# Performance work log

Measured on AMD Instinct MI355X. Metric: run time of the kernel, lower is better.

The kernel has to match this reference:

```python
import jax, jax.numpy as jnp
import numpy as np

POOL = 7; SR = 2; SCALE = 1.0 / 16
NUM_CLASSES = 21
NMS_THR = 0.5; MIN_SIZE = 1.0; TOPK = 100; SCORE_THR = 0.05
BBOX_CLIP = float(np.log(1000.0 / 16))


def roi_align(feat, rois):
    # feat: [C,H,W]; rois: [P,4] xyxy in image coords. torchvision aligned=True, sampling_ratio=2.
    C, H, W = feat.shape
    S = POOL * SR
    x0r = rois[:, 0] * SCALE - 0.5
    y0r = rois[:, 1] * SCALE - 0.5
    bw = (rois[:, 2] - rois[:, 0]) * SCALE / POOL
    bh = (rois[:, 3] - rois[:, 1]) * SCALE / POOL
    t = (jnp.arange(S, dtype=feat.dtype) + 0.5) / SR  # sample offsets in bin units
    ys = y0r[:, None] + bh[:, None] * t  # [P,S]
    xs = x0r[:, None] + bw[:, None] * t  # [P,S]
    vy = (ys >= -1.0) & (ys <= H)
    vx = (xs >= -1.0) & (xs <= W)
    y = jnp.clip(ys, 0.0, H - 1)
    x = jnp.clip(xs, 0.0, W - 1)
    yl = jnp.floor(y).astype(jnp.int32); xl = jnp.floor(x).astype(jnp.int32)
    yh = jnp.minimum(yl + 1, H - 1);     xh = jnp.minimum(xl + 1, W - 1)
    ly = y - yl; lx = x - xl
    hy = 1.0 - ly; hx = 1.0 - lx

    def g(Yi, Xi):  # -> [C,P,S,S]
        return feat[:, Yi[:, :, None], Xi[:, None, :]]

    val = (g(yl, xl) * (hy[:, :, None] * hx[:, None, :])
         + g(yl, xh) * (hy[:, :, None] * lx[:, None, :])
         + g(yh, xl) * (ly[:, :, None] * hx[:, None, :])
         + g(yh, xh) * (ly[:, :, None] * lx[:, None, :]))
    val = val * (vy[:, :, None] & vx[:, None, :])[None].astype(feat.dtype)
    P = rois.shape[0]
    val = val.reshape(C, P, POOL, SR, POOL, SR).mean(axis=(3, 5))  # avg over 2x2 samples/bin
    return val.transpose(1, 0, 2, 3)  # [P,C,POOL,POOL]


def decode(pred, proposals):
    # pred: [N,K,4] (dx,dy,dw,dh); proposals: [N,4]
    w = proposals[:, 2] - proposals[:, 0]
    h = proposals[:, 3] - proposals[:, 1]
    cx = proposals[:, 0] + 0.5 * w
    cy = proposals[:, 1] + 0.5 * h
    dx, dy = pred[..., 0], pred[..., 1]
    dw = jnp.minimum(pred[..., 2], BBOX_CLIP)
    dh = jnp.minimum(pred[..., 3], BBOX_CLIP)
    pcx = dx * w[:, None] + cx[:, None]
    pcy = dy * h[:, None] + cy[:, None]
    pw = jnp.exp(dw) * w[:, None]
    ph = jnp.exp(dh) * h[:, None]
    return jnp.stack([pcx - 0.5 * pw, pcy - 0.5 * ph, pcx + 0.5 * pw, pcy + 0.5 * ph], axis=-1)


def box_iou(b):
    x1, y1, x2, y2 = b[:, 0], b[:, 1], b[:, 2], b[:, 3]
    area = (x2 - x1) * (y2 - y1)
    iw = jnp.maximum(jnp.minimum(x2[:, None], x2[None, :]) - jnp.maximum(x1[:, None], x1[None, :]), 0.0)
    ih = jnp.maximum(jnp.minimum(y2[:, None], y2[None, :]) - jnp.maximum(y1[:, None], y1[None, :]), 0.0)
    inter = iw * ih
    return inter / (area[:, None] + area[None, :] - inter)


def filter_predictions(boxes, labels, scores):
    # score threshold + min-size + per-class greedy NMS + topK, static shapes (padded to TOPK)
    N = scores.shape[0]
    ws = boxes[:, 2] - boxes[:, 0]
    hs = boxes[:, 3] - boxes[:, 1]
    valid = (scores > SCORE_THR) & (ws >= MIN_SIZE) & (hs >= MIN_SIZE)
    skey = jnp.where(valid, scores, -jnp.inf)
    order = jnp.argsort(-skey)
    b = boxes[order]; s = skey[order]; l = labels[order]; v = valid[order]
    # batched_nms via per-class coordinate offset
    off = jax.lax.stop_gradient(jnp.max(boxes) + 1.0)
    ob = jax.lax.stop_gradient(b) + (l.astype(b.dtype) * off)[:, None]
    iou = box_iou(ob)  # [N,N]
    idx = jnp.arange(N)

    def body(keep, i):
        sup = (iou[i] > NMS_THR) & keep[i] & (idx > i)
        return keep & ~sup, None

    keep, _ = jax.lax.scan(body, v, idx)
    rank = jnp.cumsum(keep) - 1
    final = keep & (rank < TOPK)
    pick = jnp.argsort(jnp.where(final, idx, N))[:TOPK]  # kept indices in score order, padded
    ok = final[pick]
    out_boxes = jnp.where(ok[:, None], b[pick], 0.0)
    out_scores = jnp.where(ok, s[pick], 0.0)
    out_labels = jnp.where(ok, l[pick], -1)
    return out_boxes, out_labels, out_scores


def roi_head_forward(image, feat, proposals, fc6_w, fc6_b, fc7_w, fc7_b, cls_w, cls_b, reg_w, reg_b):
    H_img, W_img = image.shape[-2], image.shape[-1]
    pooled = roi_align(feat[0], proposals)  # [P,C,7,7]
    x = pooled.reshape(pooled.shape[0], -1)
    x = jax.nn.relu(x @ fc6_w.T + fc6_b)
    x = jax.nn.relu(x @ fc7_w.T + fc7_b)
    cls_scores = x @ cls_w.T + cls_b                       # [P,K]
    box_pred = (x @ reg_w.T + reg_b).reshape(-1, NUM_CLASSES, 4)
    boxes = decode(box_pred, proposals)                    # [P,K,4]
    scores = jax.nn.softmax(cls_scores, axis=-1)
    boxes = jnp.stack([boxes[..., 0].clip(0, W_img), boxes[..., 1].clip(0, H_img),
                       boxes[..., 2].clip(0, W_img), boxes[..., 3].clip(0, H_img)], axis=-1)
    labels = jnp.broadcast_to(jnp.arange(NUM_CLASSES), scores.shape)
    boxes = boxes[:, 1:].reshape(-1, 4)
    scores = scores[:, 1:].reshape(-1)
    labels = (labels[:, 1:] - 1).reshape(-1)
    return filter_predictions(boxes, labels, scores)


def setup_inputs() -> dict:
    key = jax.random.key(0)
    ks = jax.random.split(key, 12)
    H_img, W_img = 800, 1072
    P, C = 300, 512
    image = jnp.zeros((1, 3, H_img, W_img), jnp.float32)
    feat = jax.random.normal(ks[0], (1, C, H_img // 16, W_img // 16), jnp.float32)
    cx = jax.random.uniform(ks[1], (P,)) * W_img
    cy = jax.random.uniform(ks[2], (P,)) * H_img
    bw = 20.0 + jax.random.uniform(ks[3], (P,)) * 300.0
    bh = 20.0 + jax.random.uniform(ks[4], (P,)) * 300.0
    proposals = jnp.stack([jnp.clip(cx - bw / 2, 0, W_img), jnp.clip(cy - bh / 2, 0, H_img),
                           jnp.clip(cx + bw / 2, 0, W_img), jnp.clip(cy + bh / 2, 0, H_img)], axis=1)
    fin = C * POOL * POOL  # 25088
    D = 1024
    fc6_w = jax.random.normal(ks[5], (D, fin), jnp.float32) / np.sqrt(fin)
    fc6_b = jnp.zeros((D,), jnp.float32)
    fc7_w = jax.random.normal(ks[6], (D, D), jnp.float32) / np.sqrt(D)
    fc7_b = jnp.zeros((D,), jnp.float32)
    cls_w = jax.random.normal(ks[7], (NUM_CLASSES, D), jnp.float32) / np.sqrt(D)
    cls_b = jnp.zeros((NUM_CLASSES,), jnp.float32)
    reg_w = jax.random.normal(ks[8], (NUM_CLASSES * 4, D), jnp.float32) * 0.001
    reg_b = jnp.zeros((NUM_CLASSES * 4,), jnp.float32)
    return {"image": image, "feat": feat, "proposals": proposals,
            "fc6_w": fc6_w, "fc6_b": fc6_b, "fc7_w": fc7_w, "fc7_b": fc7_b,
            "cls_w": cls_w, "cls_b": cls_b, "reg_w": reg_w, "reg_b": reg_b}


def reference(image, feat, proposals, fc6_w, fc6_b, fc7_w, fc7_b, cls_w, cls_b, reg_w, reg_b):
    return roi_head_forward(image, feat, proposals, fc6_w, fc6_b, fc7_w, fc7_b, cls_w, cls_b, reg_w, reg_b)
```

## Files before the change

### kernel.cpp

```cpp
#include <hip/hip_runtime.h>
#include <hip/hip_bf16.h>
#include <math.h>

#define P_N   300
#define C_N   512
#define H_F   50
#define W_F   67
#define HW_F  3350
#define D_N   1024
#define FIN   25088
#define NCLS  21
#define NCAND 6000
#define W_IMG 1072.0f
#define H_IMG 800.0f
#define BBOX_CLIP_F 4.135166556742356f
#define KS6   42
#define STEPS6_PER_Z 19
#define KS7   16
#define STEPS7_PER_Z 2
#define KSH   16
#define STEPSH_PER_Z 2
#define NHEAD 128
#define NW    96
#define LO_SCALE 2048.0f
#define LO_INV   (1.0f/2048.0f)

typedef __attribute__((ext_vector_type(8)))  _Float16 half8;
typedef __attribute__((ext_vector_type(16))) float    f32x16;

__device__ __forceinline__ void split16(float f, _Float16& h, _Float16& l) {
  h = (_Float16)f;
  l = (_Float16)((f - (float)h) * LO_SCALE);
}

__global__ __launch_bounds__(256) void transpose_feat(const float* __restrict__ feat,
                                                      float* __restrict__ ft) {
  __shared__ float tile[32][33];
  const int s0 = blockIdx.x * 32, c0 = blockIdx.y * 32;
  const int tx = threadIdx.x, ty = threadIdx.y;
  for (int r = ty; r < 32; r += 8) {
    int c = c0 + r, s = s0 + tx;
    tile[r][tx] = (s < HW_F) ? feat[(size_t)c * HW_F + s] : 0.0f;
  }
  __syncthreads();
  for (int r = ty; r < 32; r += 8) {
    int s = s0 + r, c = c0 + tx;
    if (s < HW_F) ft[(size_t)s * C_N + c] = tile[tx][r];
  }
}

__global__ __launch_bounds__(256) void roi_align_k(const float* __restrict__ ft,
                                                   const float* __restrict__ rois,
                                                   _Float16* __restrict__ Xhi,
                                                   _Float16* __restrict__ Xlo) {
  __shared__ _Float16 hbuf[12544] __attribute__((aligned(16)));
  __shared__ _Float16 lbuf[12544] __attribute__((aligned(16)));
  __shared__ int   g_yl[14], g_yh[14], g_xl[14], g_xh[14];
  __shared__ float g_ly[14], g_hy[14], g_lx[14], g_hx[14];
  __shared__ int   g_vy[14], g_vx[14];

  const int p   = blockIdx.x;
  const int ch  = blockIdx.y;
  const int tid = threadIdx.x;

  if (tid < 14) {
    const float rx0 = rois[p*4+0], ry0 = rois[p*4+1], rx1 = rois[p*4+2], ry1 = rois[p*4+3];
    const float x0r = rx0 * 0.0625f - 0.5f;
    const float y0r = ry0 * 0.0625f - 0.5f;
    const float bw  = (rx1 - rx0) * 0.0625f * (1.0f / 7.0f);
    const float bh  = (ry1 - ry0) * 0.0625f * (1.0f / 7.0f);
    const float t   = ((float)tid + 0.5f) * 0.5f;

    const float ys = y0r + bh * t;
    g_vy[tid] = (ys >= -1.0f) && (ys <= (float)H_F);
    float y = fminf(fmaxf(ys, 0.0f), (float)(H_F - 1));
    int yi = (int)floorf(y);
    g_yl[tid] = yi; g_yh[tid] = min(yi + 1, H_F - 1);
    g_ly[tid] = y - (float)yi; g_hy[tid] = 1.0f - (y - (float)yi);

    const float xs = x0r + bw * t;
    g_vx[tid] = (xs >= -1.0f) && (xs <= (float)W_F);
    float x = fminf(fmaxf(xs, 0.0f), (float)(W_F - 1));
    int xi = (int)floorf(x);
    g_xl[tid] = xi; g_xh[tid] = min(xi + 1, W_F - 1);
    g_lx[tid] = x - (float)xi; g_hx[tid] = 1.0f - (x - (float)xi);
  }
  __syncthreads();

  const int c = ch * 256 + tid;
  for (int cell = 0; cell < 49; ++cell) {
    const int py = cell / 7;
    const int px = cell - py * 7;
    float acc = 0.0f;
#pragma unroll
    for (int sy = 0; sy < 2; ++sy) {
      const int iy = 2 * py + sy;
      if (!g_vy[iy]) continue;
      const float ly = g_ly[iy], hy = g_hy[iy];
      const int ry0i = g_yl[iy] * W_F, ry1i = g_yh[iy] * W_F;
#pragma unroll
      for (int sx = 0; sx < 2; ++sx) {
        const int ix = 2 * px + sx;
        if (!g_vx[ix]) continue;
        const float lx = g_lx[ix], hx = g_hx[ix];
        const float* b00 = ft + (size_t)(ry0i + g_xl[ix]) * C_N;
        const float* b01 = ft + (size_t)(ry0i + g_xh[ix]) * C_N;
        const float* b10 = ft + (size_t)(ry1i + g_xl[ix]) * C_N;
        const float* b11 = ft + (size_t)(ry1i + g_xh[ix]) * C_N;
        acc += (hy*hx)*b00[c] + (hy*lx)*b01[c] + (ly*hx)*b10[c] + (ly*lx)*b11[c];
      }
    }
    _Float16 h, l;
    split16(acc * 0.25f, h, l);
    hbuf[tid * 49 + cell] = h;
    lbuf[tid * 49 + cell] = l;
  }
  __syncthreads();

  const size_t base = (size_t)p * FIN + (size_t)ch * 12544;
  const uint4* hs = (const uint4*)hbuf;
  const uint4* ls = (const uint4*)lbuf;
  uint4* dh = (uint4*)(Xhi + base);
  uint4* dl = (uint4*)(Xlo + base);
  for (int k = tid; k < 1568; k += 256) { dh[k] = hs[k]; dl[k] = ls[k]; }
}

__device__ __forceinline__ int swz(int slot, int ks) {
  return slot ^ ((slot >> 5) & 1) ^ (((slot >> 3) & 1) << 1) ^ ((ks & 1) << 2);
}

__global__ __launch_bounds__(256, 2) void gemm_f16_3p(
    const _Float16* __restrict__ Ahi, const _Float16* __restrict__ Alo,
    const float* __restrict__ Wt, float* __restrict__ Pt,
    int M, int K, int steps_per_z, int ldc)
{
  __shared__ _Float16 lds[16384];
  const int tid  = threadIdx.x;
  const int lane = tid & 63, wave = tid >> 6;
  const int wm = wave >> 1, wn = wave & 1;

  const int GX = gridDim.x, GY = gridDim.y;
  const int T  = GX * GY * gridDim.z;
  int flat = blockIdx.x + GX * (blockIdx.y + GY * blockIdx.z);
  if ((T & 7) == 0) flat = (flat & 7) * (T >> 3) + (flat >> 3);
  const int bx = flat % GX;
  const int by = (flat / GX) % GY;
  const int bz = flat / (GX * GY);

  const int m0 = bx * 128, n0 = by * 128;
  const int steps_total = K >> 5;
  const int s0 = bz * steps_per_z;
  const int s1 = min(s0 + steps_per_z, steps_total);

  f32x16 acc0[2][2], acc1[2][2];
#pragma unroll
  for (int a = 0; a < 2; ++a)
#pragma unroll
    for (int b = 0; b < 2; ++b) {
#pragma unroll
      for (int r = 0; r < 16; ++r) { acc0[a][b][r] = 0.f; acc1[a][b][r] = 0.f; }
    }

  const int srow = tid >> 2;
  const int j8   = tid & 3;
  const int ksW  = j8 >> 1, kc8 = j8 & 1;
  const int wslot = swz((kc8 << 5) | (srow & 31), ksW);

  for (int step = s0; step < s1; ++step) {
    const int kb = step << 5;
#pragma unroll
    for (int half = 0; half < 2; ++half) {
      const int row = srow + half * 64;
      const int mf  = row >> 5;
      const int gm  = m0 + row;
      uint4 vh = make_uint4(0,0,0,0), vl = make_uint4(0,0,0,0);
      if (gm < M) {
        vh = *reinterpret_cast<const uint4*>(Ahi + (size_t)gm * K + kb + j8 * 8);
        vl = *reinterpret_cast<const uint4*>(Alo + (size_t)gm * K + kb + j8 * 8);
      }
      const int base = (mf * 2 + ksW) * 512 + wslot * 8;
      *reinterpret_cast<uint4*>(&lds[base])        = vh;
      *reinterpret_cast<uint4*>(&lds[4096 + base]) = vl;
    }
#pragma unroll
    for (int half = 0; half < 2; ++half) {
      const int n = srow + half * 64;
      const float* wp = Wt + (size_t)(n0 + n) * K + kb + j8 * 8;
      const float4 f0 = *reinterpret_cast<const float4*>(wp);
      const float4 f1 = *reinterpret_cast<const float4*>(wp + 4);
      float fv[8] = {f0.x, f0.y, f0.z, f0.w, f1.x, f1.y, f1.z, f1.w};
      union { _Float16 h[8]; uint4 v; } uh, ul;
#pragma unroll
      for (int e = 0; e < 8; ++e) split16(fv[e], uh.h[e], ul.h[e]);
      const int nf = n >> 5;
      const int base = 8192 + (nf * 2 + ksW) * 512 + wslot * 8;
      *reinterpret_cast<uint4*>(&lds[base])        = uh.v;
      *reinterpret_cast<uint4*>(&lds[4096 + base]) = ul.v;
    }
    __syncthreads();
#pragma unroll
    for (int ks = 0; ks < 2; ++ks) {
      const int rslot = swz(lane, ks) * 8;
      half8 ah[2], al[2], bh[2], bl[2];
#pragma unroll
      for (int mi = 0; mi < 2; ++mi) {
        const int mf = wm * 2 + mi;
        ah[mi] = *reinterpret_cast<const half8*>(&lds[(mf * 2 + ks) * 512 + rslot]);
        al[mi] = *reinterpret_cast<const half8*>(&lds[4096 + (mf * 2 + ks) * 512 + rslot]);
      }
#pragma unroll
      for (int ni = 0; ni < 2; ++ni) {
        const int nf = wn * 2 + ni;
        bh[ni] = *reinterpret_cast<const half8*>(&lds[8192  + (nf * 2 + ks) * 512 + rslot]);
        bl[ni] = *reinterpret_cast<const half8*>(&lds[12288 + (nf * 2 + ks) * 512 + rslot]);
      }
#pragma unroll
      for (int mi = 0; mi < 2; ++mi)
#pragma unroll
        for (int ni = 0; ni < 2; ++ni) {
          acc0[mi][ni] = __builtin_amdgcn_mfma_f32_32x32x16_f16(ah[mi], bh[ni], acc0[mi][ni], 0, 0, 0);
          acc1[mi][ni] = __builtin_amdgcn_mfma_f32_32x32x16_f16(ah[mi], bl[ni], acc1[mi][ni], 0, 0, 0);
          acc1[mi][ni] = __builtin_amdgcn_mfma_f32_32x32x16_f16(al[mi], bh[ni], acc1[mi][ni], 0, 0, 0);
        }
    }
    __syncthreads();
  }
  const int col = lane & 31, rhi = lane >> 5;
  float* outp = Pt + (size_t)bz * ((size_t)M * ldc);
#pragma unroll
  for (int mi = 0; mi < 2; ++mi)
#pragma unroll
    for (int ni = 0; ni < 2; ++ni) {
      const int n = n0 + (wn * 2 + ni) * 32 + col;
      if (n >= ldc) continue;
#pragma unroll
      for (int r = 0; r < 16; ++r) {
        const int m = m0 + (wm * 2 + mi) * 32 + ((r & 3) + 8 * (r >> 2) + 4 * rhi);
        if (m < M) outp[(size_t)m * ldc + n] = acc0[mi][ni][r] + acc1[mi][ni][r] * LO_INV;
      }
    }
}

__global__ __launch_bounds__(256) void reduce_bias(
    const float* __restrict__ Pt, const float* __restrict__ bias,
    float* __restrict__ out_f32, _Float16* __restrict__ out_hi, _Float16* __restrict__ out_lo,
    int MN, int KS, int nmask, int relu)
{
  int i = blockIdx.x * 256 + threadIdx.x;
  if (i >= MN) return;
  float s = 0.0f;
  for (int k = 0; k < KS; ++k) s += Pt[(size_t)k * MN + i];
  s += bias[i & nmask];
  if (relu) s = fmaxf(s, 0.0f);
  if (out_f32) out_f32[i] = s;
  if (out_hi) {
    _Float16 h, l; split16(s, h, l);
    out_hi[i] = h; out_lo[i] = l;
  }
}

__global__ __launch_bounds__(256) void prep_head(const float* __restrict__ cls_w,
                                                 const float* __restrict__ cls_b,
                                                 const float* __restrict__ reg_w,
                                                 const float* __restrict__ reg_b,
                                                 float* __restrict__ Wpad,
                                                 float* __restrict__ bpad) {
  const int row = blockIdx.x;
  const int t = threadIdx.x;
  const float* src = (row < NCLS) ? (cls_w + (size_t)row * D_N)
                   : (row < 105)  ? (reg_w + (size_t)(row - NCLS) * D_N) : nullptr;
  float4 v = make_float4(0.f, 0.f, 0.f, 0.f);
  if (src) v = reinterpret_cast<const float4*>(src)[t];
  reinterpret_cast<float4*>(Wpad + (size_t)row * D_N)[t] = v;
  if (t == 0)
    bpad[row] = (row < NCLS) ? cls_b[row] : (row < 105) ? reg_b[row - NCLS] : 0.0f;
}

__global__ __launch_bounds__(64) void decode_kernel(const float* __restrict__ logits,
                                                    const float* __restrict__ props,
                                                    float* __restrict__ cboxes,
                                                    float* __restrict__ cscores,
                                                    int* __restrict__ cvalid) {
  const int p = blockIdx.x;
  const int lane = threadIdx.x;
  const float* lg = logits + (size_t)p * NHEAD;

  float s = (lane < NCLS) ? lg[lane] : -__builtin_inff();
  float mx = s;
#pragma unroll
  for (int off = 32; off > 0; off >>= 1) mx = fmaxf(mx, __shfl_xor(mx, off));
  float e = (lane < NCLS) ? expf(s - mx) : 0.0f;
  float sum = e;
#pragma unroll
  for (int off = 32; off > 0; off >>= 1) sum += __shfl_xor(sum, off);
  const float sm = e / sum;

  if (lane >= 1 && lane < NCLS) {
    const int c = lane;
    const float x0 = props[p*4+0], y0 = props[p*4+1], x1 = props[p*4+2], y1 = props[p*4+3];
    const float w = x1 - x0, hh = y1 - y0;
    const float cx = x0 + 0.5f * w, cy = y0 + 0.5f * hh;
    const float dx = lg[NCLS + c*4 + 0];
    const float dy = lg[NCLS + c*4 + 1];
    const float dw = fminf(lg[NCLS + c*4 + 2], BBOX_CLIP_F);
    const float dh = fminf(lg[NCLS + c*4 + 3], BBOX_CLIP_F);
    const float pcx = dx * w + cx, pcy = dy * hh + cy;
    const float pw = expf(dw) * w, ph = expf(dh) * hh;
    float bx0 = pcx - 0.5f * pw, by0 = pcy - 0.5f * ph;
    float bx1 = pcx + 0.5f * pw, by1 = pcy + 0.5f * ph;
    bx0 = fminf(fmaxf(bx0, 0.0f), W_IMG);
    by0 = fminf(fmaxf(by0, 0.0f), H_IMG);
    bx1 = fminf(fmaxf(bx1, 0.0f), W_IMG);
    by1 = fminf(fmaxf(by1, 0.0f), H_IMG);
    const int idx = p * 20 + (c - 1);
    cboxes[idx*4+0] = bx0; cboxes[idx*4+1] = by0;
    cboxes[idx*4+2] = bx1; cboxes[idx*4+3] = by1;
    const bool valid = (sm > 0.05f) && ((bx1 - bx0) >= 1.0f) && ((by1 - by0) >= 1.0f);
    cscores[idx] = sm;
    cvalid[idx] = valid ? 1 : 0;
  }
}

__global__ void zero_counter(int* c) { if (threadIdx.x == 0 && blockIdx.x == 0) *c = 0; }

__global__ __launch_bounds__(256) void compact_kernel(const float* __restrict__ cscores,
                                                      const int* __restrict__ cvalid,
                                                      unsigned long long* __restrict__ ckeys,
                                                      int* __restrict__ vcount) {
  int i = blockIdx.x * 256 + threadIdx.x;
  if (i >= NCAND) return;
  if (cvalid[i]) {
    int pos = atomicAdd(vcount, 1);
    unsigned u = __float_as_uint(cscores[i]);
    ckeys[pos] = ((unsigned long long)(~u) << 32) | (unsigned)i;
  }
}

__global__ __launch_bounds__(1024) void sort_gather(const unsigned long long* __restrict__ ckeys,
                                                    const int* __restrict__ vcount,
                                                    const float* __restrict__ cboxes,
                                                    float4* __restrict__ sbox,
                                                    float* __restrict__ sscore,
                                                    int* __restrict__ slab) {
  __shared__ unsigned long long keys[8192];
  const int tid = threadIdx.x;
  const int V = *vcount;
  int Npad = 64; while (Npad < V) Npad <<= 1;
  for (int i = tid; i < Npad; i += 1024)
    keys[i] = (i < V) ? ckeys[i] : ~0ULL;
  __syncthreads();
  for (int kk = 2; kk <= Npad; kk <<= 1) {
    for (int j = kk >> 1; j > 0; j >>= 1) {
      for (int i = tid; i < Npad; i += 1024) {
        int ij = i ^ j;
        if (ij > i) {
          unsigned long long a = keys[i], b = keys[ij];
          bool up = ((i & kk) == 0);
          if ((a > b) == up) { keys[i] = b; keys[ij] = a; }
        }
      }
      __syncthreads();
    }
  }
  for (int i = tid; i < V; i += 1024) {
    unsigned long long key = keys[i];
    int idx = (int)(key & 0xffffffffu);
    sbox[i]   = *reinterpret_cast<const float4*>(&cboxes[(size_t)idx * 4]);
    sscore[i] = __uint_as_float(~(unsigned)(key >> 32));
    slab[i]   = idx % 20;
  }
}

__global__ __launch_bounds__(256) void iou_matrix(const float4* __restrict__ sbox,
                                                  const int* __restrict__ slab,
                                                  const int* __restrict__ vcount,
                                                  unsigned long long* __restrict__ mask) {
  const int V = *vcount;
  const int i = blockIdx.x * 4 + (threadIdx.x >> 6);
  const int lane = threadIdx.x & 63;
  if (i >= V) return;
  const float4 bi = sbox[i];
  const int li = slab[i];
  const float ai = (bi.z - bi.x) * (bi.w - bi.y);
  const int nw = (V + 63) >> 6;
  for (int w = 0; w < nw; ++w) {
    const int j = (w << 6) + lane;
    bool sup = false;
    if (j > i && j < V && slab[j] == li) {
      const float4 bj = sbox[j];
      const float iw = fminf(bi.z, bj.z) - fmaxf(bi.x, bj.x);
      const float ih = fminf(bi.w, bj.w) - fmaxf(bi.y, bj.y);
      const float inter = fmaxf(iw, 0.0f) * fmaxf(ih, 0.0f);
      const float aj = (bj.z - bj.x) * (bj.w - bj.y);
      sup = inter / (ai + aj - inter) > 0.5f;
    }
    const unsigned long long m = __ballot(sup);
    if (lane == 0) mask[(size_t)i * NW + w] = m;
  }
}

__global__ __launch_bounds__(64) void nms_scan(const float4* __restrict__ sbox,
                                               const float* __restrict__ sscore,
                                               const int* __restrict__ slab,
                                               const int* __restrict__ vcount,
                                               const unsigned long long* __restrict__ mask,
                                               float* __restrict__ out) {
  const int lane = threadIdx.x;
  const int V = min(*vcount, NCAND);
  unsigned long long live0 = ~0ULL, live1 = ~0ULL;
  int nk = 0;
  for (int i = 0; i < V && nk < 100; ++i) {
    const int wi = i >> 6, bi = i & 63;
    union { unsigned long long u; uint2 v; } t;
    t.u = (wi < 64) ? live0 : live1;
    const int src = (wi < 64) ? wi : (wi - 64);
    const unsigned lo = __shfl(t.v.x, src);
    const unsigned hi = __shfl(t.v.y, src);
    const unsigned long long wv = ((unsigned long long)hi << 32) | lo;
    if ((wv >> bi) & 1ULL) {
      if (lane == 0) {
        const float4 bb = sbox[i];
        out[nk*4+0] = bb.x; out[nk*4+1] = bb.y; out[nk*4+2] = bb.z; out[nk*4+3] = bb.w;
        out[400 + nk] = (float)slab[i];
        out[500 + nk] = sscore[i];
      }
      const unsigned long long* mrow = mask + (size_t)i * NW;
      live0 &= ~mrow[lane];
      if (lane < NW - 64) live1 &= ~mrow[64 + lane];
      nk++;
    }
  }
  for (int r = nk + lane; r < 100; r += 64) {
    out[r*4+0] = 0.0f; out[r*4+1] = 0.0f; out[r*4+2] = 0.0f; out[r*4+3] = 0.0f;
    out[400 + r] = -1.0f;
    out[500 + r] = 0.0f;
  }
}

extern "C" void kernel_launch(void* const* d_in, const int* in_sizes, int n_in,
                              void* d_out, int out_size, void* d_ws, size_t ws_size,
                              hipStream_t stream) {
  const float* feat   = (const float*)d_in[1];
  const float* props  = (const float*)d_in[2];
  const float* fc6_w  = (const float*)d_in[3];
  const float* fc6_b  = (const float*)d_in[4];
  const float* fc7_w  = (const float*)d_in[5];
  const float* fc7_b  = (const float*)d_in[6];
  const float* cls_w  = (const float*)d_in[7];
  const float* cls_b  = (const float*)d_in[8];
  const float* reg_w  = (const float*)d_in[9];
  const float* reg_b  = (const float*)d_in[10];

  char* ws = (char*)d_ws;
  size_t off = 0;
  auto alloc = [&](size_t bytes) -> void* {
    void* p = ws + off;
    off += (bytes + 255) & ~(size_t)255;
    return p;
  };

  _Float16* Xhi  = (_Float16*)alloc((size_t)P_N * FIN * 2);
  _Float16* Xlo  = (_Float16*)alloc((size_t)P_N * FIN * 2);
  float*    Pt   = (float*)alloc((size_t)KS6 * P_N * D_N * 4);
  _Float16* h6hi = (_Float16*)alloc((size_t)P_N * D_N * 2);
  _Float16* h6lo = (_Float16*)alloc((size_t)P_N * D_N * 2);
  _Float16* h7hi = (_Float16*)alloc((size_t)P_N * D_N * 2);
  _Float16* h7lo = (_Float16*)alloc((size_t)P_N * D_N * 2);
  float*    Wpad = (float*)alloc((size_t)NHEAD * D_N * 4);
  float*    bpad = (float*)alloc((size_t)NHEAD * 4);
  float*  logits = (float*)alloc((size_t)P_N * NHEAD * 4);
  float*  cboxes = (float*)alloc((size_t)NCAND * 4 * 4);
  float* cscores = (float*)alloc((size_t)NCAND * 4);
  int*    cvalid = (int*)alloc((size_t)NCAND * 4);
  unsigned long long* ckeys = (unsigned long long*)alloc((size_t)NCAND * 8);
  float4*   sbox = (float4*)alloc((size_t)NCAND * 16);
  float*  sscore = (float*)alloc((size_t)NCAND * 4);
  int*      slab = (int*)alloc((size_t)NCAND * 4);
  unsigned long long* supmask = (unsigned long long*)alloc((size_t)NCAND * NW * 8);
  int*    vcount = (int*)alloc(256);
  float* ft = Pt;
  (void)ws_size; (void)in_sizes; (void)n_in; (void)out_size;

  prep_head<<<NHEAD, 256, 0, stream>>>(cls_w, cls_b, reg_w, reg_b, Wpad, bpad);
  transpose_feat<<<dim3((HW_F + 31) / 32, C_N / 32), dim3(32, 8), 0, stream>>>(feat, ft);
  roi_align_k<<<dim3(P_N, 2), 256, 0, stream>>>(ft, props, Xhi, Xlo);
  gemm_f16_3p<<<dim3(3, 8, KS6), 256, 0, stream>>>(Xhi, Xlo, fc6_w, Pt, P_N, FIN, STEPS6_PER_Z, D_N);
  reduce_bias<<<(P_N * D_N + 255) / 256, 256, 0, stream>>>(
      Pt, fc6_b, nullptr, h6hi, h6lo, P_N * D_N, KS6, D_N - 1, 1);
  gemm_f16_3p<<<dim3(3, 8, KS7), 256, 0, stream>>>(h6hi, h6lo, fc7_w, Pt, P_N, D_N, STEPS7_PER_Z, D_N);
  reduce_bias<<<(P_N * D_N + 255) / 256, 256, 0, stream>>>(
      Pt, fc7_b, nullptr, h7hi, h7lo, P_N * D_N, KS7, D_N - 1, 1);
  gemm_f16_3p<<<dim3(3, 1, KSH), 256, 0, stream>>>(h7hi, h7lo, Wpad, Pt, P_N, D_N, STEPSH_PER_Z, NHEAD);
  reduce_bias<<<(P_N * NHEAD + 255) / 256, 256, 0, stream>>>(
      Pt, bpad, logits, nullptr, nullptr, P_N * NHEAD, KSH, NHEAD - 1, 0);
  decode_kernel<<<P_N, 64, 0, stream>>>(logits, props, cboxes, cscores, cvalid);
  zero_counter<<<1, 1, 0, stream>>>(vcount);
  compact_kernel<<<(NCAND + 255) / 256, 256, 0, stream>>>(cscores, cvalid, ckeys, vcount);
  sort_gather<<<1, 1024, 0, stream>>>(ckeys, vcount, cboxes, sbox, sscore, slab);
  iou_matrix<<<(NCAND + 3) / 4, 256, 0, stream>>>(sbox, slab, vcount, supmask);
  nms_scan<<<1, 64, 0, stream>>>(sbox, sscore, slab, vcount, supmask, (float*)d_out);
}
```

Before: 344.9 us.

## Merge split-fp16 accumulators, fuse compaction into decode, speed NMS scan

The split-fp16 GEMM now pre-scales the A and B operands so that the hi and lo cross products can share a single accumulator set. This halves accumulator registers and lets launch bounds ask for 3 blocks per CU. Candidate compaction and the counter reset are folded into decode_kernel and prep_head, which removes two kernel launches and the intermediate score and valid buffers. nms_scan now walks only live bits with ffs and reads only the mask words it needs. The risks are reduced accuracy from fp16 range/scaling choices and a nondeterministic candidate order when atomics are used inside decode, which the sort should absorb.

```diff
diff --git a/kernel.cpp b/kernel.cpp
--- a/kernel.cpp
+++ b/kernel.cpp
@@ -22,15 +22,17 @@
 #define STEPSH_PER_Z 2
 #define NHEAD 128
 #define NW    96
-#define LO_SCALE 2048.0f
-#define LO_INV   (1.0f/2048.0f)
+#define A_SCALE 16.0f
+#define B_SCALE 256.0f
+#define O_SCALE (1.0f / 4096.0f)
 
 typedef __attribute__((ext_vector_type(8)))  _Float16 half8;
 typedef __attribute__((ext_vector_type(16))) float    f32x16;
 
-__device__ __forceinline__ void split16(float f, _Float16& h, _Float16& l) {
-  h = (_Float16)f;
-  l = (_Float16)((f - (float)h) * LO_SCALE);
+__device__ __forceinline__ void splitA(float f, _Float16& h, _Float16& l) {
+  float fs = f * A_SCALE;
+  h = (_Float16)fs;
+  l = (_Float16)(fs - (float)h);
 }
 
 __global__ __launch_bounds__(256) void transpose_feat(const float* __restrict__ feat,
@@ -111,7 +113,7 @@
       }
     }
     _Float16 h, l;
-    split16(acc * 0.25f, h, l);
+    splitA(acc * 0.25f, h, l);
     hbuf[tid * 49 + cell] = h;
     lbuf[tid * 49 + cell] = l;
   }
@@ -129,7 +131,7 @@
   return slot ^ ((slot >> 5) & 1) ^ (((slot >> 3) & 1) << 1) ^ ((ks & 1) << 2);
 }
 
-__global__ __launch_bounds__(256, 2) void gemm_f16_3p(
+__global__ __launch_bounds__(256, 3) void gemm_f16_3p(
     const _Float16* __restrict__ Ahi, const _Float16* __restrict__ Alo,
     const float* __restrict__ Wt, float* __restrict__ Pt,
     int M, int K, int steps_per_z, int ldc)
@@ -152,14 +154,13 @@
   const int s0 = bz * steps_per_z;
   const int s1 = min(s0 + steps_per_z, steps_total);
 
-  f32x16 acc0[2][2], acc1[2][2];
+  f32x16 acc[2][2];
 #pragma unroll
   for (int a = 0; a < 2; ++a)
 #pragma unroll
-    for (int b = 0; b < 2; ++b) {
-#pragma unroll
-      for (int r = 0; r < 16; ++r) { acc0[a][b][r] = 0.f; acc1[a][b][r] = 0.f; }
-    }
+    for (int b = 0; b < 2; ++b)
+#pragma unroll
+      for (int r = 0; r < 16; ++r) acc[a][b][r] = 0.f;
 
   const int srow = tid >> 2;
   const int j8   = tid & 3;
@@ -191,7 +192,11 @@
       float fv[8] = {f0.x, f0.y, f0.z, f0.w, f1.x, f1.y, f1.z, f1.w};
       union { _Float16 h[8]; uint4 v; } uh, ul;
 #pragma unroll
-      for (int e = 0; e < 8; ++e) split16(fv[e], uh.h[e], ul.h[e]);
+      for (int e = 0; e < 8; ++e) {
+        float fs = fv[e] * B_SCALE;
+        uh.h[e] = (_Float16)fs;
+        ul.h[e] = (_Float16)(fs - (float)uh.h[e]);
+      }
       const int nf = n >> 5;
       const int base = 8192 + (nf * 2 + ksW) * 512 + wslot * 8;
       *reinterpret_cast<uint4*>(&lds[base])        = uh.v;
@@ -218,9 +223,9 @@
       for (int mi = 0; mi < 2; ++mi)
 #pragma unroll
         for (int ni = 0; ni < 2; ++ni) {
-          acc0[mi][ni] = __builtin_amdgcn_mfma_f32_32x32x16_f16(ah[mi], bh[ni], acc0[mi][ni], 0, 0, 0);
-          acc1[mi][ni] = __builtin_amdgcn_mfma_f32_32x32x16_f16(ah[mi], bl[ni], acc1[mi][ni], 0, 0, 0);
-          acc1[mi][ni] = __builtin_amdgcn_mfma_f32_32x32x16_f16(al[mi], bh[ni], acc1[mi][ni], 0, 0, 0);
+          acc[mi][ni] = __builtin_amdgcn_mfma_f32_32x32x16_f16(ah[mi], bh[ni], acc[mi][ni], 0, 0, 0);
+          acc[mi][ni] = __builtin_amdgcn_mfma_f32_32x32x16_f16(ah[mi], bl[ni], acc[mi][ni], 0, 0, 0);
+          acc[mi][ni] = __builtin_amdgcn_mfma_f32_32x32x16_f16(al[mi], bh[ni], acc[mi][ni], 0, 0, 0);
         }
     }
     __syncthreads();
@@ -236,7 +241,7 @@
 #pragma unroll
       for (int r = 0; r < 16; ++r) {
         const int m = m0 + (wm * 2 + mi) * 32 + ((r & 3) + 8 * (r >> 2) + 4 * rhi);
-        if (m < M) outp[(size_t)m * ldc + n] = acc0[mi][ni][r] + acc1[mi][ni][r] * LO_INV;
+        if (m < M) outp[(size_t)m * ldc + n] = acc[mi][ni][r] * O_SCALE;
       }
     }
 }
@@ -254,7 +259,7 @@
   if (relu) s = fmaxf(s, 0.0f);
   if (out_f32) out_f32[i] = s;
   if (out_hi) {
-    _Float16 h, l; split16(s, h, l);
+    _Float16 h, l; splitA(s, h, l);
     out_hi[i] = h; out_lo[i] = l;
   }
 }
@@ -264,9 +269,11 @@
                                                  const float* __restrict__ reg_w,
                                                  const float* __restrict__ reg_b,
                                                  float* __restrict__ Wpad,
-                                                 float* __restrict__ bpad) {
+                                                 float* __restrict__ bpad,
+                                                 int* __restrict__ vcount) {
   const int row = blockIdx.x;
   const int t = threadIdx.x;
+  if (row == 0 && t == 0) *vcount = 0;
   const float* src = (row < NCLS) ? (cls_w + (size_t)row * D_N)
                    : (row < 105)  ? (reg_w + (size_t)(row - NCLS) * D_N) : nullptr;
   float4 v = make_float4(0.f, 0.f, 0.f, 0.f);
@@ -279,8 +286,8 @@
 __global__ __launch_bounds__(64) void decode_kernel(const float* __restrict__ logits,
                                                     const float* __restrict__ props,
                                                     float* __restrict__ cboxes,
-                                                    float* __restrict__ cscores,
-                                                    int* __restrict__ cvalid) {
+                                                    unsigned long long* __restrict__ ckeys,
+                                                    int* __restrict__ vcount) {
   const int p = blockIdx.x;
   const int lane = threadIdx.x;
   const float* lg = logits + (size_t)p * NHEAD;
@@ -316,23 +323,11 @@
     cboxes[idx*4+0] = bx0; cboxes[idx*4+1] = by0;
     cboxes[idx*4+2] = bx1; cboxes[idx*4+3] = by1;
     const bool valid = (sm > 0.05f) && ((bx1 - bx0) >= 1.0f) && ((by1 - by0) >= 1.0f);
-    cscores[idx] = sm;
-    cvalid[idx] = valid ? 1 : 0;
-  }
-}
-
-__global__ void zero_counter(int* c) { if (threadIdx.x == 0 && blockIdx.x == 0) *c = 0; }
-
-__global__ __launch_bounds__(256) void compact_kernel(const float* __restrict__ cscores,
-                                                      const int* __restrict__ cvalid,
-                                                      unsigned long long* __restrict__ ckeys,
-                                                      int* __restrict__ vcount) {
-  int i = blockIdx.x * 256 + threadIdx.x;
-  if (i >= NCAND) return;
-  if (cvalid[i]) {
-    int pos = atomicAdd(vcount, 1);
-    unsigned u = __float_as_uint(cscores[i]);
-    ckeys[pos] = ((unsigned long long)(~u) << 32) | (unsigned)i;
+    if (valid) {
+      int pos = atomicAdd(vcount, 1);
+      unsigned u = __float_as_uint(sm);
+      ckeys[pos] = ((unsigned long long)(~u) << 32) | (unsigned)idx;
+    }
   }
 }
 
@@ -399,6 +394,16 @@
   }
 }
 
+__device__ __forceinline__ unsigned long long bcast_live(unsigned long long live0,
+                                                         unsigned long long live1, int w) {
+  union { unsigned long long u; uint2 v; } t;
+  t.u = (w < 64) ? live0 : live1;
+  const int src = w & 63;
+  const unsigned lo = __shfl(t.v.x, src);
+  const unsigned hi = __shfl(t.v.y, src);
+  return ((unsigned long long)hi << 32) | lo;
+}
+
 __global__ __launch_bounds__(64) void nms_scan(const float4* __restrict__ sbox,
                                                const float* __restrict__ sscore,
                                                const int* __restrict__ slab,
@@ -407,17 +412,16 @@
                                                float* __restrict__ out) {
   const int lane = threadIdx.x;
   const int V = min(*vcount, NCAND);
+  const int nw = (V + 63) >> 6;
   unsigned long long live0 = ~0ULL, live1 = ~0ULL;
   int nk = 0;
-  for (int i = 0; i < V && nk < 100; ++i) {
-    const int wi = i >> 6, bi = i & 63;
-    union { unsigned long long u; uint2 v; } t;
-    t.u = (wi < 64) ? live0 : live1;
-    const int src = (wi < 64) ? wi : (wi - 64);
-    const unsigned lo = __shfl(t.v.x, src);
-    const unsigned hi = __shfl(t.v.y, src);
-    const unsigned long long wv = ((unsigned long long)hi << 32) | lo;
-    if ((wv >> bi) & 1ULL) {
+  for (int w = 0; w < nw && nk < 100; ++w) {
+    const int nb = V - (w << 6);
+    const unsigned long long vmask = (nb >= 64) ? ~0ULL : ((1ULL << nb) - 1ULL);
+    unsigned long long wv = bcast_live(live0, live1, w) & vmask;
+    while (wv && nk < 100) {
+      const int b = __ffsll((long long)wv) - 1;
+      const int i = (w << 6) + b;
       if (lane == 0) {
         const float4 bb = sbox[i];
         out[nk*4+0] = bb.x; out[nk*4+1] = bb.y; out[nk*4+2] = bb.z; out[nk*4+3] = bb.w;
@@ -425,9 +429,11 @@
         out[500 + nk] = sscore[i];
       }
       const unsigned long long* mrow = mask + (size_t)i * NW;
-      live0 &= ~mrow[lane];
-      if (lane < NW - 64) live1 &= ~mrow[64 + lane];
+      if (lane < nw) live0 &= ~mrow[lane];
+      if (64 + lane < nw) live1 &= ~mrow[64 + lane];
       nk++;
+      wv = bcast_live(live0, live1, w) & vmask;
+      wv &= (b == 63) ? 0ULL : ~((2ULL << b) - 1ULL);
     }
   }
   for (int r = nk + lane; r < 100; r += 64) {
@@ -470,8 +476,6 @@
   float*    bpad = (float*)alloc((size_t)NHEAD * 4);
   float*  logits = (float*)alloc((size_t)P_N * NHEAD * 4);
   float*  cboxes = (float*)alloc((size_t)NCAND * 4 * 4);
-  float* cscores = (float*)alloc((size_t)NCAND * 4);
-  int*    cvalid = (int*)alloc((size_t)NCAND * 4);
   unsigned long long* ckeys = (unsigned long long*)alloc((size_t)NCAND * 8);
   float4*   sbox = (float4*)alloc((size_t)NCAND * 16);
   float*  sscore = (float*)alloc((size_t)NCAND * 4);
@@ -481,7 +485,7 @@
   float* ft = Pt;
   (void)ws_size; (void)in_sizes; (void)n_in; (void)out_size;
 
-  prep_head<<<NHEAD, 256, 0, stream>>>(cls_w, cls_b, reg_w, reg_b, Wpad, bpad);
+  prep_head<<<NHEAD, 256, 0, stream>>>(cls_w, cls_b, reg_w, reg_b, Wpad, bpad, vcount);
   transpose_feat<<<dim3((HW_F + 31) / 32, C_N / 32), dim3(32, 8), 0, stream>>>(feat, ft);
   roi_align_k<<<dim3(P_N, 2), 256, 0, stream>>>(ft, props, Xhi, Xlo);
   gemm_f16_3p<<<dim3(3, 8, KS6), 256, 0, stream>>>(Xhi, Xlo, fc6_w, Pt, P_N, FIN, STEPS6_PER_Z, D_N);
@@ -493,9 +497,7 @@
   gemm_f16_3p<<<dim3(3, 1, KSH), 256, 0, stream>>>(h7hi, h7lo, Wpad, Pt, P_N, D_N, STEPSH_PER_Z, NHEAD);
   reduce_bias<<<(P_N * NHEAD + 255) / 256, 256, 0, stream>>>(
       Pt, bpad, logits, nullptr, nullptr, P_N * NHEAD, KSH, NHEAD - 1, 0);
-  decode_kernel<<<P_N, 64, 0, stream>>>(logits, props, cboxes, cscores, cvalid);
-  zero_counter<<<1, 1, 0, stream>>>(vcount);
-  compact_kernel<<<(NCAND + 255) / 256, 256, 0, stream>>>(cscores, cvalid, ckeys, vcount);
+  decode_kernel<<<P_N, 64, 0, stream>>>(logits, props, cboxes, ckeys, vcount);
   sort_gather<<<1, 1024, 0, stream>>>(ckeys, vcount, cboxes, sbox, sscore, slab);
   iou_matrix<<<(NCAND + 3) / 4, 256, 0, stream>>>(sbox, slab, vcount, supmask);
   nms_scan<<<1, 64, 0, stream>>>(sbox, sscore, slab, vcount, supmask, (float*)d_out);
```

New measurement: 343.2 us. Within noise of the previous version (-0.5%).
